# Kernel optimization log

Hardware: AMD Instinct MI355X
Metric: run time of the kernel (lower is better)

Reference implementation:

```python
import jax, jax.numpy as jnp
import numpy as np
from jax import lax

INT8_NARROW = (-127.0, 127.0)   # brevitas Int8WeightPerTensorFloat (narrow range)
INT8_FULL = (-128.0, 127.0)     # brevitas Int8ActPerTensorFloat
INT32 = (-2.0**31, 2.0**31 - 1)


def _fake_quant(v, scale, qmin, qmax):
    # round-to-nearest, clip, dequant (per-tensor)
    return jnp.clip(jnp.round(v / scale), qmin, qmax) * scale


def _conv(x, w, stride):
    return lax.conv_general_dilated(
        x, w, window_strides=(stride, stride), padding=[(1, 1), (1, 1)],
        dimension_numbers=("NCHW", "OIHW", "NCHW"))


def setup_inputs() -> dict:
    key = jax.random.key(0)
    ks = jax.random.split(key, 5)
    B, Cin, Cout, H = 64, 256, 512, 28
    x = jax.random.normal(ks[0], (B, Cin, H, H), dtype=jnp.float32)
    w1 = jax.random.normal(ks[1], (Cout, Cin, 3, 3), dtype=jnp.float32) * 0.05
    b1 = jax.random.normal(ks[2], (Cout,), dtype=jnp.float32) * 0.01
    w2 = jax.random.normal(ks[3], (Cout, Cout, 3, 3), dtype=jnp.float32) * 0.05
    b2 = jax.random.normal(ks[4], (Cout,), dtype=jnp.float32) * 0.01
    return {
        "x": x, "w1": w1, "b1": b1, "w2": w2, "b2": b2,
        "in_scale": jnp.full((1,), 0.05, dtype=jnp.float32),
        "act1_scale": jnp.full((1,), 0.05, dtype=jnp.float32),
        "act2_scale": jnp.full((1,), 0.05, dtype=jnp.float32),
    }


def reference(x, w1, b1, w2, b2, in_scale, act1_scale, act2_scale):
    s_in = in_scale[0]
    s_a1 = act1_scale[0]
    s_a2 = act2_scale[0]

    # conv1: per-tensor int8 weight fake-quant (max-abs stats, narrow range)
    s_w1 = jnp.max(jnp.abs(w1)) / 127.0
    wq1 = _fake_quant(w1, s_w1, *INT8_NARROW)
    bq1 = _fake_quant(b1, s_in * s_w1, *INT32)  # Int32Bias: scale = in_scale*w_scale
    out = _conv(x, wq1, 2) + bq1[None, :, None, None]

    # act1: int8 activation fake-quant (learned per-tensor scale)
    out = _fake_quant(out, s_a1, *INT8_FULL)

    # conv2
    s_w2 = jnp.max(jnp.abs(w2)) / 127.0
    wq2 = _fake_quant(w2, s_w2, *INT8_NARROW)
    bq2 = _fake_quant(b2, s_a1 * s_w2, *INT32)
    out = _conv(out, wq2, 1) + bq2[None, :, None, None]

    # act2
    out = _fake_quant(out, s_a2, *INT8_FULL)
    return out
```

## Files before the change

kernel.cpp:

```cpp
#include <hip/hip_runtime.h>

typedef int i32x4 __attribute__((ext_vector_type(4)));

__device__ __forceinline__ void gl_lds16(const signed char* g, signed char* l) {
    __builtin_amdgcn_global_load_lds(
        (const __attribute__((address_space(1))) void*)g,
        (__attribute__((address_space(3))) void*)l, 16, 0, 0);
}

#define XQ_SCALE 2048.0f
#define XQ_DELTA (1.0f / 2048.0f)

__global__ void init_ws_kernel(unsigned* p) {
    if (threadIdx.x < 2) p[threadIdx.x] = 0u;
}

__global__ void absmax2_kernel(const float* __restrict__ w1, const float* __restrict__ w2,
                               unsigned* __restrict__ out) {
    const bool second = blockIdx.x >= 256;
    const float* w = second ? w2 : w1;
    const int n4 = second ? (512 * 512 * 9 / 4) : (512 * 256 * 9 / 4);
    unsigned* o = out + (second ? 1 : 0);
    float m = 0.0f;
    for (int i = (blockIdx.x & 255) * 256 + threadIdx.x; i < n4; i += 65536) {
        float4 v = ((const float4*)w)[i];
        m = fmaxf(m, fmaxf(fmaxf(fabsf(v.x), fabsf(v.y)), fmaxf(fabsf(v.z), fabsf(v.w))));
    }
#pragma unroll
    for (int off = 32; off > 0; off >>= 1)
        m = fmaxf(m, __shfl_down(m, off));
    if ((threadIdx.x & 63) == 0)
        atomicMax(o, __float_as_uint(m));
}

__global__ void prep_kernel(const float* __restrict__ w1, const float* __restrict__ w2,
                            const float* __restrict__ b1, const float* __restrict__ b2,
                            const unsigned* __restrict__ absbits,
                            const float* __restrict__ in_scale, const float* __restrict__ act1_scale,
                            signed char* __restrict__ wq1, signed char* __restrict__ wq2,
                            float* __restrict__ bq1, float* __restrict__ bq2,
                            signed char* __restrict__ xhi, signed char* __restrict__ xlo,
                            signed char* __restrict__ act) {
    constexpr int N1 = 512 * 2304;
    constexpr int N2 = 512 * 4608;
    constexpr int NB = 1024;
    constexpr int XH = 64 * 900 * 16;
    constexpr int AH = 64 * 256 * 32;
    int idx = blockIdx.x * blockDim.x + threadIdx.x;
    const uint4 z = {0, 0, 0, 0};
    if (idx < N1) {
        const int n = idx / 2304;
        const int k = idx - n * 2304;
        const int r = k >> 8;
        const int cin = k & 255;
        const int kh = r / 3;
        const int kw = r - kh * 3;
        const float s = __uint_as_float(absbits[0]) * (1.0f / 127.0f);
        const float v = w1[((n * 256 + cin) * 3 + kh) * 3 + kw];
        float q = rintf(v / s);
        q = fminf(fmaxf(q, -127.0f), 127.0f);
        wq1[idx] = (signed char)(int)q;
    } else if ((idx -= N1) < N2) {
        const int n = idx / 4608;
        const int k = idx - n * 4608;
        const int r = k >> 9;
        const int cin = k & 511;
        const int kh = r / 3;
        const int kw = r - kh * 3;
        const float s = __uint_as_float(absbits[1]) * (1.0f / 127.0f);
        const float v = w2[((n * 512 + cin) * 3 + kh) * 3 + kw];
        float q = rintf(v / s);
        q = fminf(fmaxf(q, -127.0f), 127.0f);
        wq2[idx] = (signed char)(int)q;
    } else if ((idx -= N2) < NB) {
        if (idx < 512) {
            const float s = (*in_scale) * (__uint_as_float(absbits[0]) * (1.0f / 127.0f));
            float q = rintf(b1[idx] / s);
            q = fminf(fmaxf(q, -2147483648.0f), 2147483648.0f);
            bq1[idx] = q * s;
        } else {
            const int j = idx - 512;
            const float s = (*act1_scale) * (__uint_as_float(absbits[1]) * (1.0f / 127.0f));
            float q = rintf(b2[j] / s);
            q = fminf(fmaxf(q, -2147483648.0f), 2147483648.0f);
            bq2[j] = q * s;
        }
    } else if ((idx -= NB) < XH) {
        const int b = idx / (900 * 16);
        const int r = idx - b * (900 * 16);
        const int pos = r >> 4;
        const int ch = r & 15;
        const int h = pos / 30;
        const int w = pos - h * 30;
        if (h == 0 || h == 29 || w == 0 || w == 29) {
            const int off = (b * 900 + pos) * 256 + ch * 16;
            *(uint4*)(xhi + off) = z;
            *(uint4*)(xlo + off) = z;
        }
    } else if ((idx -= XH) < AH) {
        const int b = idx / (256 * 32);
        const int r = idx - b * (256 * 32);
        const int pos = r >> 5;
        const int ch = r & 31;
        const int h = pos >> 4;
        const int w = pos & 15;
        if (h == 0 || h == 15 || w == 0 || w == 15) {
            const int off = (b * 256 + pos) * 512 + ch * 16;
            *(uint4*)(act + off) = z;
        }
    }
}

__global__ __launch_bounds__(256) void xform_x_kernel(const float* __restrict__ x,
                                                      signed char* __restrict__ hi,
                                                      signed char* __restrict__ lo) {
    __shared__ float t[32][33];
    const int tx = threadIdx.x & 31;
    const int ty = threadIdx.x >> 5;
    const int b = blockIdx.z;
    const int c0 = blockIdx.y * 32;
    const int hw0 = blockIdx.x * 32;
#pragma unroll
    for (int i = 0; i < 4; ++i) {
        const int c = c0 + ty + i * 8;
        const int hw = hw0 + tx;
        float v = 0.0f;
        if (hw < 784) v = x[(b * 256 + c) * 784 + hw];
        t[ty + i * 8][tx] = v;
    }
    __syncthreads();
    if (threadIdx.x < 128) {
        const int hw_l = threadIdx.x >> 2;
        const int cg = (threadIdx.x & 3) * 8;
        const int hw = hw0 + hw_l;
        if (hw < 784) {
            union { signed char c[8]; uint2 u; } ph, pl;
#pragma unroll
            for (int j = 0; j < 8; ++j) {
                const float v = t[cg + j][hw_l];
                int q = (int)rintf(v * XQ_SCALE);
                q = max(-16383, min(16383, q));
                ph.c[j] = (signed char)(q >> 7);
                pl.c[j] = (signed char)(q & 127);
            }
            const int r = hw / 28;
            const int o = (b * 900 + (r + 1) * 30 + (hw - r * 28) + 1) * 256 + c0 + cg;
            *(uint2*)&hi[o] = ph.u;
            *(uint2*)&lo[o] = pl.u;
        }
    }
}

template<int CIN, int STRIDE, int HP, int HOUT, bool SPLIT, bool FINAL>
__global__ __launch_bounds__(128, 2) void conv_gemm_kernel(
    const signed char* __restrict__ Ahi,
    const signed char* __restrict__ Alo,
    const signed char* __restrict__ Wt,
    const float* __restrict__ bias,
    const unsigned* __restrict__ wabs,
    const float* __restrict__ s_pre,
    const float* __restrict__ s_act,
    signed char* __restrict__ act_out,
    float* __restrict__ out_final)
{
    constexpr int K = 9 * CIN;
    constexpr int HW = HOUT * HOUT;
    constexpr int LOG2CIN = (CIN == 256) ? 8 : 9;
    constexpr int NACC = SPLIT ? 8 : 4;

    __shared__ __align__(16) signed char As[64 * 128];
    __shared__ __align__(16) signed char As2[SPLIT ? 64 * 128 : 16];
    __shared__ __align__(16) signed char Bs[128 * 128];

    const int tid = threadIdx.x;
    const int lane = tid & 63;
    const int wv = tid >> 6;
    const int quad = lane >> 4;
    const int l16 = lane & 15;
    const int m0 = blockIdx.y * 64;
    const int n0 = blockIdx.x * 128;

    const int lrow = lane >> 3;
    const int koff = ((lane & 7) ^ lrow) * 16;

    int aoff[8];
    int boff[16];
    if (wv == 0) {
#pragma unroll
        for (int c = 0; c < 8; ++c) {
            const int r = c * 8 + lrow;
            const int m = m0 + r;
            const int b = m / HW;
            const int rem = m - b * HW;
            const int oh = rem / HOUT;
            const int ow = rem - oh * HOUT;
            aoff[c] = ((b * HP + oh * STRIDE) * HP + ow * STRIDE) * CIN + koff;
        }
    } else {
#pragma unroll
        for (int c = 0; c < 16; ++c)
            boff[c] = (n0 + c * 8 + lrow) * K + koff;
    }

    i32x4 acc[NACC][4];
#pragma unroll
    for (int mi = 0; mi < NACC; ++mi)
#pragma unroll
        for (int ni = 0; ni < 4; ++ni)
            acc[mi][ni] = i32x4{0, 0, 0, 0};

    for (int k0 = 0; k0 < K; k0 += 128) {
        const int r9 = k0 >> LOG2CIN;
        const int c0k = k0 & (CIN - 1);
        const int kh = r9 / 3;
        const int kw = r9 - kh * 3;
        const int ashift = (kh * HP + kw) * CIN + c0k;

        __syncthreads();
        if (wv == 0) {
#pragma unroll
            for (int c = 0; c < 8; ++c) {
                gl_lds16(Ahi + aoff[c] + ashift, &As[c * 1024]);
                if constexpr (SPLIT) gl_lds16(Alo + aoff[c] + ashift, &As2[c * 1024]);
            }
        } else {
#pragma unroll
            for (int c = 0; c < 16; ++c)
                gl_lds16(Wt + boff[c] + k0, &Bs[c * 1024]);
        }
        __syncthreads();

#pragma unroll
        for (int ks = 0; ks < 2; ++ks) {
            i32x4 af[NACC];
            i32x4 bfr[4];
#pragma unroll
            for (int mi = 0; mi < 4; ++mi) {
                const int row = mi * 16 + l16;
                const int sl = ((ks * 4 + quad) ^ (row & 7)) * 16;
                af[mi] = *(const i32x4*)&As[row * 128 + sl];
                if constexpr (SPLIT)
                    af[mi + 4] = *(const i32x4*)&As2[row * 128 + sl];
            }
#pragma unroll
            for (int ni = 0; ni < 4; ++ni) {
                const int row = wv * 64 + ni * 16 + l16;
                const int sl = ((ks * 4 + quad) ^ (row & 7)) * 16;
                bfr[ni] = *(const i32x4*)&Bs[row * 128 + sl];
            }
#pragma unroll
            for (int mi = 0; mi < 4; ++mi)
#pragma unroll
                for (int ni = 0; ni < 4; ++ni) {
                    acc[mi][ni] = __builtin_amdgcn_mfma_i32_16x16x64_i8(af[mi], bfr[ni], acc[mi][ni], 0, 0, 0);
                    if constexpr (SPLIT)
                        acc[mi + 4][ni] = __builtin_amdgcn_mfma_i32_16x16x64_i8(af[mi + 4], bfr[ni], acc[mi + 4][ni], 0, 0, 0);
                }
        }
    }

    float alpha = __uint_as_float(*wabs) * (1.0f / 127.0f);
    if (FINAL) alpha *= *s_pre;
    if (SPLIT) alpha *= XQ_DELTA;
    const float sact = *s_act;

    float bv[4];
#pragma unroll
    for (int ni = 0; ni < 4; ++ni)
        bv[ni] = bias[n0 + wv * 64 + ni * 16 + l16];

#pragma unroll
    for (int mi = 0; mi < 4; ++mi) {
#pragma unroll
        for (int i = 0; i < 4; ++i) {
            const int m = m0 + mi * 16 + quad * 4 + i;
            const int b = m / HW;
            const int rem = m - b * HW;
            const int oh = rem / HOUT;
            const int ow = rem - oh * HOUT;
#pragma unroll
            for (int ni = 0; ni < 4; ++ni) {
                const int col = n0 + wv * 64 + ni * 16 + l16;
                int tot = acc[mi][ni][i];
                if constexpr (SPLIT) tot = tot * 128 + acc[mi + 4][ni][i];
                const float v = (float)tot * alpha + bv[ni];
                float q = rintf(v / sact);
                q = fminf(fmaxf(q, -128.0f), 127.0f);
                if (FINAL) {
                    out_final[(b * 512 + col) * HW + oh * HOUT + ow] = q * sact;
                } else {
                    act_out[(b * 256 + (oh + 1) * 16 + (ow + 1)) * 512 + col] = (signed char)(int)q;
                }
            }
        }
    }
}

extern "C" void kernel_launch(void* const* d_in, const int* in_sizes, int n_in,
                              void* d_out, int out_size, void* d_ws, size_t ws_size,
                              hipStream_t stream) {
    const float* x  = (const float*)d_in[0];
    const float* w1 = (const float*)d_in[1];
    const float* b1 = (const float*)d_in[2];
    const float* w2 = (const float*)d_in[3];
    const float* b2 = (const float*)d_in[4];
    const float* in_scale   = (const float*)d_in[5];
    const float* act1_scale = (const float*)d_in[6];
    const float* act2_scale = (const float*)d_in[7];
    float* out = (float*)d_out;

    char* ws = (char*)d_ws;
    unsigned* absbits = (unsigned*)(ws + 0);
    float* bq1 = (float*)(ws + 64);
    float* bq2 = (float*)(ws + 2112);
    signed char* wq1 = (signed char*)(ws + 8192);
    signed char* wq2 = (signed char*)(ws + 1187840);
    signed char* xhi = (signed char*)(ws + 3547136);
    signed char* xlo = (signed char*)(ws + 18292736);
    signed char* act = (signed char*)(ws + 33038336);

    init_ws_kernel<<<1, 64, 0, stream>>>(absbits);
    absmax2_kernel<<<512, 256, 0, stream>>>(w1, w2, absbits);

    constexpr int PREP_TOTAL = 512 * 2304 + 512 * 4608 + 1024 + 64 * 900 * 16 + 64 * 256 * 32;
    prep_kernel<<<(PREP_TOTAL + 255) / 256, 256, 0, stream>>>(
        w1, w2, b1, b2, absbits, in_scale, act1_scale, wq1, wq2, bq1, bq2, xhi, xlo, act);

    xform_x_kernel<<<dim3(25, 8, 64), 256, 0, stream>>>(x, xhi, xlo);

    conv_gemm_kernel<256, 2, 30, 14, true, false><<<dim3(4, 196), 128, 0, stream>>>(
        xhi, xlo, wq1, bq1, absbits, act1_scale, act1_scale, act, nullptr);

    conv_gemm_kernel<512, 1, 16, 14, false, true><<<dim3(4, 196), 128, 0, stream>>>(
        act, nullptr, wq2, bq2, absbits + 1, act1_scale, act2_scale, nullptr, out);
}
```

Measured before the change: 261.0 us.

## Use four waves per conv GEMM block and fuse prep with input transform

The conv GEMM kernels move from 128 to 256 threads per block. Each wave now covers a 32x64 sub-tile instead of 64x64, and all waves share the global-to-LDS loads rather than splitting them into an A-loader wave and a B-loader wave. The goal is more waves in flight to hide memory latency and fewer accumulator registers per wave. The prep kernel is merged with the input int8 split transform. It writes weights as 16-byte vectors and only launches threads for border pixels when zeroing padding, which removes one launch and most idle threads. In exchange, the block loses some register-level reuse of the B fragments, and the launch bounds add register pressure constraints.

```diff
diff --git a/kernel.cpp b/kernel.cpp
--- a/kernel.cpp
+++ b/kernel.cpp
@@ -33,46 +33,59 @@
         atomicMax(o, __float_as_uint(m));
 }
 
-__global__ void prep_kernel(const float* __restrict__ w1, const float* __restrict__ w2,
-                            const float* __restrict__ b1, const float* __restrict__ b2,
-                            const unsigned* __restrict__ absbits,
-                            const float* __restrict__ in_scale, const float* __restrict__ act1_scale,
-                            signed char* __restrict__ wq1, signed char* __restrict__ wq2,
-                            float* __restrict__ bq1, float* __restrict__ bq2,
-                            signed char* __restrict__ xhi, signed char* __restrict__ xlo,
-                            signed char* __restrict__ act) {
-    constexpr int N1 = 512 * 2304;
-    constexpr int N2 = 512 * 4608;
-    constexpr int NB = 1024;
-    constexpr int XH = 64 * 900 * 16;
-    constexpr int AH = 64 * 256 * 32;
-    int idx = blockIdx.x * blockDim.x + threadIdx.x;
+__global__ __launch_bounds__(256) void prep_all_kernel(
+    const float* __restrict__ x,
+    const float* __restrict__ w1, const float* __restrict__ w2,
+    const float* __restrict__ b1, const float* __restrict__ b2,
+    const unsigned* __restrict__ absbits,
+    const float* __restrict__ in_scale, const float* __restrict__ act1_scale,
+    signed char* __restrict__ wq1, signed char* __restrict__ wq2,
+    float* __restrict__ bq1, float* __restrict__ bq2,
+    signed char* __restrict__ xhi, signed char* __restrict__ xlo,
+    signed char* __restrict__ act) {
+    __shared__ float t[128][33];
+    const int blk = blockIdx.x;
+    const int tid = threadIdx.x;
     const uint4 z = {0, 0, 0, 0};
-    if (idx < N1) {
-        const int n = idx / 2304;
-        const int k = idx - n * 2304;
-        const int r = k >> 8;
-        const int cin = k & 255;
+
+    if (blk < 288) {
+        const int thr = blk * 256 + tid;
+        const int n = thr / 144;
+        const int chunk = thr - n * 144;
+        const int r = chunk >> 4;
+        const int cin0 = (chunk & 15) * 16;
         const int kh = r / 3;
         const int kw = r - kh * 3;
-        const float s = __uint_as_float(absbits[0]) * (1.0f / 127.0f);
-        const float v = w1[((n * 256 + cin) * 3 + kh) * 3 + kw];
-        float q = rintf(v / s);
-        q = fminf(fmaxf(q, -127.0f), 127.0f);
-        wq1[idx] = (signed char)(int)q;
-    } else if ((idx -= N1) < N2) {
-        const int n = idx / 4608;
-        const int k = idx - n * 4608;
-        const int r = k >> 9;
-        const int cin = k & 511;
+        const float inv_s = 127.0f / __uint_as_float(absbits[0]);
+        union { signed char c[16]; uint4 u; } pk;
+#pragma unroll
+        for (int j = 0; j < 16; ++j) {
+            const float v = w1[((n * 256 + cin0 + j) * 3 + kh) * 3 + kw];
+            float q = rintf(v * inv_s);
+            q = fminf(fmaxf(q, -127.0f), 127.0f);
+            pk.c[j] = (signed char)(int)q;
+        }
+        *(uint4*)&wq1[n * 2304 + r * 256 + cin0] = pk.u;
+    } else if (blk < 864) {
+        const int thr = (blk - 288) * 256 + tid;
+        const int n = thr / 288;
+        const int chunk = thr - n * 288;
+        const int r = chunk >> 5;
+        const int cin0 = (chunk & 31) * 16;
         const int kh = r / 3;
         const int kw = r - kh * 3;
-        const float s = __uint_as_float(absbits[1]) * (1.0f / 127.0f);
-        const float v = w2[((n * 512 + cin) * 3 + kh) * 3 + kw];
-        float q = rintf(v / s);
-        q = fminf(fmaxf(q, -127.0f), 127.0f);
-        wq2[idx] = (signed char)(int)q;
-    } else if ((idx -= N2) < NB) {
+        const float inv_s = 127.0f / __uint_as_float(absbits[1]);
+        union { signed char c[16]; uint4 u; } pk;
+#pragma unroll
+        for (int j = 0; j < 16; ++j) {
+            const float v = w2[((n * 512 + cin0 + j) * 3 + kh) * 3 + kw];
+            float q = rintf(v * inv_s);
+            q = fminf(fmaxf(q, -127.0f), 127.0f);
+            pk.c[j] = (signed char)(int)q;
+        }
+        *(uint4*)&wq2[n * 4608 + r * 512 + cin0] = pk.u;
+    } else if (blk < 868) {
+        const int idx = (blk - 864) * 256 + tid;
         if (idx < 512) {
             const float s = (*in_scale) * (__uint_as_float(absbits[0]) * (1.0f / 127.0f));
             float q = rintf(b1[idx] / s);
@@ -85,58 +98,57 @@
             q = fminf(fmaxf(q, -2147483648.0f), 2147483648.0f);
             bq2[j] = q * s;
         }
-    } else if ((idx -= NB) < XH) {
-        const int b = idx / (900 * 16);
-        const int r = idx - b * (900 * 16);
-        const int pos = r >> 4;
-        const int ch = r & 15;
-        const int h = pos / 30;
-        const int w = pos - h * 30;
-        if (h == 0 || h == 29 || w == 0 || w == 29) {
-            const int off = (b * 900 + pos) * 256 + ch * 16;
-            *(uint4*)(xhi + off) = z;
-            *(uint4*)(xlo + off) = z;
-        }
-    } else if ((idx -= XH) < AH) {
-        const int b = idx / (256 * 32);
-        const int r = idx - b * (256 * 32);
-        const int pos = r >> 5;
-        const int ch = r & 31;
-        const int h = pos >> 4;
-        const int w = pos & 15;
-        if (h == 0 || h == 15 || w == 0 || w == 15) {
-            const int off = (b * 256 + pos) * 512 + ch * 16;
-            *(uint4*)(act + off) = z;
-        }
-    }
-}
-
-__global__ __launch_bounds__(256) void xform_x_kernel(const float* __restrict__ x,
-                                                      signed char* __restrict__ hi,
-                                                      signed char* __restrict__ lo) {
-    __shared__ float t[32][33];
-    const int tx = threadIdx.x & 31;
-    const int ty = threadIdx.x >> 5;
-    const int b = blockIdx.z;
-    const int c0 = blockIdx.y * 32;
-    const int hw0 = blockIdx.x * 32;
-#pragma unroll
-    for (int i = 0; i < 4; ++i) {
-        const int c = c0 + ty + i * 8;
-        const int hw = hw0 + tx;
-        float v = 0.0f;
-        if (hw < 784) v = x[(b * 256 + c) * 784 + hw];
-        t[ty + i * 8][tx] = v;
-    }
-    __syncthreads();
-    if (threadIdx.x < 128) {
-        const int hw_l = threadIdx.x >> 2;
-        const int cg = (threadIdx.x & 3) * 8;
+    } else if (blk < 1332) {
+        const int thr = (blk - 868) * 256 + tid;
+        const int b = thr / (116 * 16);
+        const int rr = thr - b * (116 * 16);
+        const int p = rr >> 4;
+        const int ch = rr & 15;
+        int h, w;
+        if (p < 30)      { h = 0;          w = p; }
+        else if (p < 60) { h = 29;         w = p - 30; }
+        else if (p < 88) { h = p - 60 + 1; w = 0; }
+        else             { h = p - 88 + 1; w = 29; }
+        const int off = (b * 900 + h * 30 + w) * 256 + ch * 16;
+        *(uint4*)(xhi + off) = z;
+        *(uint4*)(xlo + off) = z;
+    } else if (blk < 1812) {
+        const int thr = (blk - 1332) * 256 + tid;
+        const int b = thr / (60 * 32);
+        const int rr = thr - b * (60 * 32);
+        const int p = rr >> 5;
+        const int ch = rr & 31;
+        int h, w;
+        if (p < 16)      { h = 0;          w = p; }
+        else if (p < 32) { h = 15;         w = p - 16; }
+        else if (p < 46) { h = p - 32 + 1; w = 0; }
+        else             { h = p - 46 + 1; w = 15; }
+        const int off = (b * 256 + h * 16 + w) * 512 + ch * 16;
+        *(uint4*)(act + off) = z;
+    } else {
+        const int xb = blk - 1812;
+        const int hwb = xb % 25;
+        const int rest = xb / 25;
+        const int cb = rest & 1;
+        const int b = rest >> 1;
+        const int c0 = cb * 128;
+        const int hw0 = hwb * 32;
+#pragma unroll
+        for (int ci = 0; ci < 16; ++ci) {
+            const int crow = (tid >> 5) + ci * 8;
+            const int hw = hw0 + (tid & 31);
+            float v = 0.0f;
+            if (hw < 784) v = x[(b * 256 + c0 + crow) * 784 + hw];
+            t[crow][tid & 31] = v;
+        }
+        __syncthreads();
+        const int hw_l = tid >> 3;
+        const int cg = (tid & 7) * 16;
         const int hw = hw0 + hw_l;
         if (hw < 784) {
-            union { signed char c[8]; uint2 u; } ph, pl;
-#pragma unroll
-            for (int j = 0; j < 8; ++j) {
+            union { signed char c[16]; uint4 u; } ph, pl;
+#pragma unroll
+            for (int j = 0; j < 16; ++j) {
                 const float v = t[cg + j][hw_l];
                 int q = (int)rintf(v * XQ_SCALE);
                 q = max(-16383, min(16383, q));
@@ -145,14 +157,14 @@
             }
             const int r = hw / 28;
             const int o = (b * 900 + (r + 1) * 30 + (hw - r * 28) + 1) * 256 + c0 + cg;
-            *(uint2*)&hi[o] = ph.u;
-            *(uint2*)&lo[o] = pl.u;
+            *(uint4*)&xhi[o] = ph.u;
+            *(uint4*)&xlo[o] = pl.u;
         }
     }
 }
 
 template<int CIN, int STRIDE, int HP, int HOUT, bool SPLIT, bool FINAL>
-__global__ __launch_bounds__(128, 2) void conv_gemm_kernel(
+__global__ __launch_bounds__(256, 3) void conv_gemm_kernel(
     const signed char* __restrict__ Ahi,
     const signed char* __restrict__ Alo,
     const signed char* __restrict__ Wt,
@@ -166,7 +178,8 @@
     constexpr int K = 9 * CIN;
     constexpr int HW = HOUT * HOUT;
     constexpr int LOG2CIN = (CIN == 256) ? 8 : 9;
-    constexpr int NACC = SPLIT ? 8 : 4;
+    constexpr int NC = SPLIT ? 8 : 6;
+    constexpr int NACC = SPLIT ? 4 : 2;
 
     __shared__ __align__(16) signed char As[64 * 128];
     __shared__ __align__(16) signed char As2[SPLIT ? 64 * 128 : 16];
@@ -175,6 +188,8 @@
     const int tid = threadIdx.x;
     const int lane = tid & 63;
     const int wv = tid >> 6;
+    const int wm = wv & 1;
+    const int wn = wv >> 1;
     const int quad = lane >> 4;
     const int l16 = lane & 15;
     const int m0 = blockIdx.y * 64;
@@ -183,23 +198,36 @@
     const int lrow = lane >> 3;
     const int koff = ((lane & 7) ^ lrow) * 16;
 
-    int aoff[8];
-    int boff[16];
-    if (wv == 0) {
-#pragma unroll
-        for (int c = 0; c < 8; ++c) {
-            const int r = c * 8 + lrow;
-            const int m = m0 + r;
+    const signed char* srcb[NC];
+    signed char* dstp[NC];
+    bool isA[NC];
+#pragma unroll
+    for (int i = 0; i < NC; ++i) {
+        const int g = wv * NC + i;
+        int atype;
+        int c;
+        if (SPLIT) {
+            atype = (g < 8) ? 0 : (g < 16 ? 1 : 2);
+            c = (g < 8) ? g : (g < 16 ? g - 8 : g - 16);
+        } else {
+            atype = (g < 8) ? 0 : 2;
+            c = (g < 8) ? g : g - 8;
+        }
+        if (atype == 2) {
+            srcb[i] = Wt + (n0 + c * 8 + lrow) * K + koff;
+            dstp[i] = &Bs[c * 1024];
+            isA[i] = false;
+        } else {
+            const int m = m0 + c * 8 + lrow;
             const int b = m / HW;
             const int rem = m - b * HW;
             const int oh = rem / HOUT;
             const int ow = rem - oh * HOUT;
-            aoff[c] = ((b * HP + oh * STRIDE) * HP + ow * STRIDE) * CIN + koff;
-        }
-    } else {
-#pragma unroll
-        for (int c = 0; c < 16; ++c)
-            boff[c] = (n0 + c * 8 + lrow) * K + koff;
+            const int off = ((b * HP + oh * STRIDE) * HP + ow * STRIDE) * CIN + koff;
+            srcb[i] = (atype == 0 ? Ahi : Alo) + off;
+            dstp[i] = (atype == 0 ? &As[c * 1024] : &As2[c * 1024]);
+            isA[i] = true;
+        }
     }
 
     i32x4 acc[NACC][4];
@@ -217,17 +245,9 @@
         const int ashift = (kh * HP + kw) * CIN + c0k;
 
         __syncthreads();
-        if (wv == 0) {
-#pragma unroll
-            for (int c = 0; c < 8; ++c) {
-                gl_lds16(Ahi + aoff[c] + ashift, &As[c * 1024]);
-                if constexpr (SPLIT) gl_lds16(Alo + aoff[c] + ashift, &As2[c * 1024]);
-            }
-        } else {
-#pragma unroll
-            for (int c = 0; c < 16; ++c)
-                gl_lds16(Wt + boff[c] + k0, &Bs[c * 1024]);
-        }
+#pragma unroll
+        for (int i = 0; i < NC; ++i)
+            gl_lds16(srcb[i] + (isA[i] ? ashift : k0), dstp[i]);
         __syncthreads();
 
 #pragma unroll
@@ -235,26 +255,26 @@
             i32x4 af[NACC];
             i32x4 bfr[4];
 #pragma unroll
-            for (int mi = 0; mi < 4; ++mi) {
-                const int row = mi * 16 + l16;
+            for (int mi = 0; mi < 2; ++mi) {
+                const int row = wm * 32 + mi * 16 + l16;
                 const int sl = ((ks * 4 + quad) ^ (row & 7)) * 16;
                 af[mi] = *(const i32x4*)&As[row * 128 + sl];
                 if constexpr (SPLIT)
-                    af[mi + 4] = *(const i32x4*)&As2[row * 128 + sl];
+                    af[mi + 2] = *(const i32x4*)&As2[row * 128 + sl];
             }
 #pragma unroll
             for (int ni = 0; ni < 4; ++ni) {
-                const int row = wv * 64 + ni * 16 + l16;
+                const int row = wn * 64 + ni * 16 + l16;
                 const int sl = ((ks * 4 + quad) ^ (row & 7)) * 16;
                 bfr[ni] = *(const i32x4*)&Bs[row * 128 + sl];
             }
 #pragma unroll
-            for (int mi = 0; mi < 4; ++mi)
+            for (int mi = 0; mi < 2; ++mi)
 #pragma unroll
                 for (int ni = 0; ni < 4; ++ni) {
                     acc[mi][ni] = __builtin_amdgcn_mfma_i32_16x16x64_i8(af[mi], bfr[ni], acc[mi][ni], 0, 0, 0);
                     if constexpr (SPLIT)
-                        acc[mi + 4][ni] = __builtin_amdgcn_mfma_i32_16x16x64_i8(af[mi + 4], bfr[ni], acc[mi + 4][ni], 0, 0, 0);
+                        acc[mi + 2][ni] = __builtin_amdgcn_mfma_i32_16x16x64_i8(af[mi + 2], bfr[ni], acc[mi + 2][ni], 0, 0, 0);
                 }
         }
     }
@@ -267,22 +287,22 @@
     float bv[4];
 #pragma unroll
     for (int ni = 0; ni < 4; ++ni)
-        bv[ni] = bias[n0 + wv * 64 + ni * 16 + l16];
-
-#pragma unroll
-    for (int mi = 0; mi < 4; ++mi) {
+        bv[ni] = bias[n0 + wn * 64 + ni * 16 + l16];
+
+#pragma unroll
+    for (int mi = 0; mi < 2; ++mi) {
 #pragma unroll
         for (int i = 0; i < 4; ++i) {
-            const int m = m0 + mi * 16 + quad * 4 + i;
+            const int m = m0 + wm * 32 + mi * 16 + quad * 4 + i;
             const int b = m / HW;
             const int rem = m - b * HW;
             const int oh = rem / HOUT;
             const int ow = rem - oh * HOUT;
 #pragma unroll
             for (int ni = 0; ni < 4; ++ni) {
-                const int col = n0 + wv * 64 + ni * 16 + l16;
+                const int col = n0 + wn * 64 + ni * 16 + l16;
                 int tot = acc[mi][ni][i];
-                if constexpr (SPLIT) tot = tot * 128 + acc[mi + 4][ni][i];
+                if constexpr (SPLIT) tot = tot * 128 + acc[mi + 2][ni][i];
                 const float v = (float)tot * alpha + bv[ni];
                 float q = rintf(v / sact);
                 q = fminf(fmaxf(q, -128.0f), 127.0f);
@@ -322,15 +342,13 @@
     init_ws_kernel<<<1, 64, 0, stream>>>(absbits);
     absmax2_kernel<<<512, 256, 0, stream>>>(w1, w2, absbits);
 
-    constexpr int PREP_TOTAL = 512 * 2304 + 512 * 4608 + 1024 + 64 * 900 * 16 + 64 * 256 * 32;
-    prep_kernel<<<(PREP_TOTAL + 255) / 256, 256, 0, stream>>>(
-        w1, w2, b1, b2, absbits, in_scale, act1_scale, wq1, wq2, bq1, bq2, xhi, xlo, act);
-
-    xform_x_kernel<<<dim3(25, 8, 64), 256, 0, stream>>>(x, xhi, xlo);
-
-    conv_gemm_kernel<256, 2, 30, 14, true, false><<<dim3(4, 196), 128, 0, stream>>>(
+    prep_all_kernel<<<5012, 256, 0, stream>>>(
+        x, w1, w2, b1, b2, absbits, in_scale, act1_scale,
+        wq1, wq2, bq1, bq2, xhi, xlo, act);
+
+    conv_gemm_kernel<256, 2, 30, 14, true, false><<<dim3(4, 196), 256, 0, stream>>>(
         xhi, xlo, wq1, bq1, absbits, act1_scale, act1_scale, act, nullptr);
 
-    conv_gemm_kernel<512, 1, 16, 14, false, true><<<dim3(4, 196), 128, 0, stream>>>(
+    conv_gemm_kernel<512, 1, 16, 14, false, true><<<dim3(4, 196), 256, 0, stream>>>(
         act, nullptr, wq2, bq2, absbits + 1, act1_scale, act2_scale, nullptr, out);
 }
```

New measurement: 265.6 us. Within noise of the previous version (+1.8%).
